# Kernel tuning notes

Measured on AMD Instinct MI355X. Metric: run time of the kernel, lower is better.

## Reference

```python
import jax, jax.numpy as jnp
import numpy as np

SR = 48000
NC = 8      # num_cylinders
NH = 64     # num_harmonics
NB = 32     # num_noisebands
B_, T_ = 2, 65536
TWO_PI = 2.0 * np.pi


def _gumbel_softmax_hard(key, logits, tau=1.0):
    g = jax.random.gumbel(key, logits.shape, dtype=logits.dtype)
    y = jax.nn.softmax((logits + g) / tau)
    hard = jax.nn.one_hot(jnp.argmax(y, axis=-1), logits.shape[-1], dtype=y.dtype)
    return hard + y - jax.lax.stop_gradient(y)  # straight-through (hard=True)


def _resonant_activation(x, min_mag):
    return jnp.sign(x) * (min_mag + (1.0 - min_mag) * jnp.abs(jnp.tanh(x)))


def _format_coefficients(one_hot, fb_gain, refl, lowpass, tau):
    shifted = jnp.roll(one_hot, 1, axis=-1)
    refl = jax.nn.sigmoid(refl) if lowpass else jnp.tanh(refl)
    k1 = _resonant_activation(refl[0], tau)
    k2 = _resonant_activation(refl[1], tau)
    a1 = k1 * (1.0 - k2)
    a2 = jnp.clip(k2, -0.999, 0.999)
    a1_bound = 0.999 - jnp.abs(a2)
    a1 = jnp.clip(a1, -a1_bound, a1_bound)
    g = jax.nn.sigmoid(fb_gain[0]) ** 0.45
    return one_hot * (a1 * g) + shifted * (a2 * g)


def _sample_wise_lpc(x, a):
    # All-pole IIR: y[t] = x[t] - sum_{i=1..P} a[t, i-1] * y[t-i]
    # x: (B,T), a: (B,T,P) -> (B,T). Inherently sequential scan over T.
    B, T = x.shape
    P = a.shape[-1]

    def step(buf, inp):          # buf: (B,P) = [y[t-1], ..., y[t-P]]
        xt, at = inp             # (B,), (B,P)
        yt = xt - jnp.sum(at * buf, axis=-1)
        buf = jnp.concatenate([yt[:, None], buf[:, :-1]], axis=1)
        return buf, yt

    buf0 = jnp.zeros((B, P), x.dtype)
    _, y = jax.lax.scan(step, buf0, (x.T, jnp.transpose(a, (1, 0, 2))))
    return y.T


def _resonator(excitation, delay_param, fb_gain, refl, min_delay, max_delay, lowpass, tau, key):
    # excitation: (B,1,T)
    sel = _gumbel_softmax_hard(key, delay_param)                 # (max-min,)
    coeffs = _format_coefficients(sel, fb_gain, refl, lowpass, tau)
    coeffs = jnp.concatenate([jnp.zeros(min_delay, coeffs.dtype), coeffs])  # (max_delay,)
    x = excitation[:, 0, :]
    B, T = x.shape
    a = jnp.broadcast_to(coeffs[None, None, :], (B, T, max_delay))
    return _sample_wise_lpc(x, a)[:, None, :]


def setup_inputs() -> dict:
    key = jax.random.key(0)
    ks = jax.random.split(key, 16)
    inp = {
        'f0': jax.random.uniform(ks[0], (B_, 1, T_), jnp.float32),
        'harmonic_amplitudes': jax.random.uniform(ks[1], (B_, NC * NH, T_), jnp.float32),
        'harmonic_fm': jax.random.uniform(ks[2], (B_, 1, T_), jnp.float32),
        'cylinder_phase_offsets': jax.random.normal(ks[3], (B_, NC, T_), jnp.float32),
        'cylinder_pulse_shapes': jax.random.uniform(ks[4], (B_, 2 * NC, T_), jnp.float32),
        'noisebank_amplitudes': jax.random.uniform(ks[5], (B_, NB, T_), jnp.float32),
        'noise_pulse_shapes': jax.random.uniform(ks[6], (B_, 2, T_), jnp.float32),
        'noise_pulse_gain': jax.random.uniform(ks[7], (B_, 1, T_), jnp.float32),
        'flow_noise_gain': jax.random.uniform(ks[8], (B_, 1, T_), jnp.float32),
        'noise_bands': jax.random.normal(ks[9], (NB, T_), jnp.float32),
        'delay_a': jax.random.normal(ks[10], (125 - 40,), jnp.float32),
        'fbgain_a': jnp.ones((1,), jnp.float32),
        'refl_a': jax.random.normal(ks[11], (2,), jnp.float32),
        'delay_b': jax.random.normal(ks[12], (125 - 40,), jnp.float32),
        'fbgain_b': jnp.ones((1,), jnp.float32),
        'refl_b': jax.random.normal(ks[13], (2,), jnp.float32),
        'delay_c': jax.random.normal(ks[14], (40 - 32,), jnp.float32),
        'fbgain_c': jnp.ones((1,), jnp.float32),
        'refl_c': jax.random.normal(ks[15], (2,), jnp.float32),
    }
    return inp


def reference(f0, harmonic_amplitudes, harmonic_fm, cylinder_phase_offsets,
              cylinder_pulse_shapes, noisebank_amplitudes, noise_pulse_shapes,
              noise_pulse_gain, flow_noise_gain, noise_bands,
              delay_a, fbgain_a, refl_a, delay_b, fbgain_b, refl_b,
              delay_c, fbgain_c, refl_c):
    B, C, T = cylinder_phase_offsets.shape
    firing_order = jnp.array([0, 4, 3, 7, 5, 2, 6, 1], dtype=f0.dtype)[:NC]
    firing_angles = firing_order / NC * TWO_PI                         # (8,)
    power_cycle_phase = jnp.cumsum(TWO_PI * f0 / SR, axis=-1) * 0.5    # (B,1,T)
    cylinder_phases = (power_cycle_phase + firing_angles[None, :, None]) % TWO_PI  # (B,8,T)

    hp = (cylinder_phases / TWO_PI) ** harmonic_fm                     # (B,8,T)
    hp = hp * TWO_PI
    harm_idx = jnp.arange(1, NH + 1, dtype=hp.dtype)
    osc = -jnp.sin(hp[:, :, None, :] * harm_idx[None, None, :, None])  # (B,8,64,T)
    amps = harmonic_amplitudes.reshape(B, NC, NH, T)
    harmonics = jnp.sum(osc * amps, axis=2)                            # (B,8,T)

    cyl_alpha = cylinder_pulse_shapes[:, :NC, :]
    cyl_beta = cylinder_pulse_shapes[:, NC:, :]
    cyl_env = (1.0 - jnp.exp(-cyl_alpha * cylinder_phases)) * jnp.exp(-cyl_beta * cylinder_phases)
    harmonics = harmonics * cyl_env * 10.0

    # NoiseBank: fixed noise bands weighted per-sample and summed over bands
    noise = jnp.einsum('bnt,nt->bt', noisebank_amplitudes, noise_bands)[:, None, :]  # (B,1,T)

    n_alpha = noise_pulse_shapes[:, 0:1, :]
    n_beta = noise_pulse_shapes[:, 1:2, :]
    noise_phase = power_cycle_phase % TWO_PI
    noise_env = (1.0 - jnp.exp(-n_alpha * noise_phase)) * jnp.exp(-n_beta * noise_phase)
    noise_bursts = noise * noise_env * noise_pulse_gain
    flow_noise = noise * flow_noise_gain * 0.3
    turbulence = harmonics * noise * (noise_pulse_gain + flow_noise_gain) * 0.7
    cylinders = harmonics + noise_bursts + flow_noise + turbulence     # (B,8,T)

    bank_a = jnp.sum(cylinders[:, :4, :], axis=1, keepdims=True)       # (B,1,T)
    bank_b = jnp.sum(cylinders[:, 4:, :], axis=1, keepdims=True)

    ka, kb, kc = jax.random.split(jax.random.key(42), 3)
    res_a = _resonator(bank_a, delay_a, fbgain_a, refl_a, 40, 125, False, 0.0, ka)
    res_b = _resonator(bank_b, delay_b, fbgain_b, refl_b, 40, 125, False, 0.0, kb)
    res_c = _resonator(res_a + res_b, delay_c, fbgain_c, refl_c, 32, 40, True, 0.0, kc)
    return jnp.sum(res_c, axis=1, keepdims=True)                       # (B,1,T)
```

## Files before the change

### kernel.cpp

```cpp
#include <hip/hip_runtime.h>
#include <cstdint>
#include <cstddef>

#define T_ 65536

__device__ __forceinline__ void tf2x32(uint32_t k0, uint32_t k1,
                                       uint32_t& x0, uint32_t& x1) {
  const uint32_t ks[3] = {k0, k1, k0 ^ k1 ^ 0x1BD11BDAu};
  const int R[8] = {13, 15, 26, 6, 17, 29, 16, 24};
  x0 += ks[0]; x1 += ks[1];
#pragma unroll
  for (int i = 0; i < 5; ++i) {
#pragma unroll
    for (int j = 0; j < 4; ++j) {
      const int r = R[(i & 1) * 4 + j];
      x0 += x1;
      x1 = (x1 << r) | (x1 >> (32 - r));
      x1 ^= x0;
    }
    x0 += ks[(i + 1) % 3];
    x1 += ks[(i + 2) % 3] + (uint32_t)(i + 1);
  }
}

__device__ __forceinline__ float gumbel_from_bits(uint32_t b) {
  float u = __uint_as_float((b >> 9) | 0x3f800000u) - 1.0f;
  u = fmaxf(u, 1.17549435e-38f);
  return -logf(-logf(u));
}

__global__ __launch_bounds__(1024) void pcp_coef_kernel(
    const float* __restrict__ f0, float* __restrict__ pcp,
    const float* __restrict__ da, const float* __restrict__ fa, const float* __restrict__ ra,
    const float* __restrict__ db, const float* __restrict__ fb, const float* __restrict__ rb,
    const float* __restrict__ dc, const float* __restrict__ fc, const float* __restrict__ rc,
    float* __restrict__ cws) {
  __shared__ double sm[1024];
  __shared__ float z[128];
  if (blockIdx.x < 2) {
    const int b = blockIdx.x;
    const int tid = threadIdx.x;
    const float* src = f0 + (size_t)b * T_;
    const int base = tid * 64;
    double loc = 0.0;
    for (int k = 0; k < 64; ++k) {
      loc += 6.283185307179586 * (double)src[base + k] / 48000.0;
    }
    sm[tid] = loc;
    __syncthreads();
    for (int off = 1; off < 1024; off <<= 1) {
      double v = (tid >= off) ? sm[tid - off] : 0.0;
      __syncthreads();
      sm[tid] += v;
      __syncthreads();
    }
    double run = (tid > 0) ? sm[tid - 1] : 0.0;
    float* dst = pcp + (size_t)b * T_;
    for (int k = 0; k < 64; ++k) {
      run += 6.283185307179586 * (double)src[base + k] / 48000.0;
      dst[base + k] = (float)(run * 0.5);
    }
  } else {
    uint32_t keys[3][2];
#pragma unroll
    for (int q = 0; q < 3; ++q) {
      uint32_t x0 = 0u, x1 = (uint32_t)q;
      tf2x32(0u, 42u, x0, x1);
      keys[q][0] = x0; keys[q][1] = x1;
    }
    const float* dl[3] = {da, db, dc};
    const float* fg[3] = {fa, fb, fc};
    const float* rf[3] = {ra, rb, rc};
    const int Ls[3] = {85, 85, 8};
    const int md[3] = {40, 40, 32};
    const int i = threadIdx.x;
    for (int r = 0; r < 3; ++r) {
      const int L = Ls[r];
      if (i < 128) z[i] = -3.4e38f;
      __syncthreads();
      if (i < L) {
        uint32_t x0 = 0u, x1 = (uint32_t)i;
        tf2x32(keys[r][0], keys[r][1], x0, x1);
        z[i] = dl[r][i] + gumbel_from_bits(x0 ^ x1);
      }
      __syncthreads();
      if (i == 0) {
        int p = 0; float best = z[0];
        for (int j = 1; j < L; ++j) { float v = z[j]; if (v > best) { best = v; p = j; } }
        const bool lowpass = (r == 2);
        float r0 = rf[r][0], r1 = rf[r][1];
        if (lowpass) { r0 = 1.f / (1.f + expf(-r0)); r1 = 1.f / (1.f + expf(-r1)); }
        else         { r0 = tanhf(r0);               r1 = tanhf(r1); }
        const float k1 = tanhf(r0), k2 = tanhf(r1);
        float a1 = k1 * (1.f - k2);
        const float a2 = fminf(fmaxf(k2, -0.999f), 0.999f);
        const float bnd = 0.999f - fabsf(a2);
        a1 = fminf(fmaxf(a1, -bnd), bnd);
        const float g = powf(1.f / (1.f + expf(-fg[r][0])), 0.45f);
        const int D1 = md[r] + p + 1;
        const int D2 = md[r] + ((p + 1) % L) + 1;
        const float C1 = a1 * g;
        const float C2 = a2 * g;
        float* cw = cws + r * 32;
        const float bin4[5] = {1.f, 4.f, 6.f, 4.f, 1.f};
        const float c1p[5] = {1.f, C1, C1*C1, C1*C1*C1, C1*C1*C1*C1};
        const float c2p[5] = {1.f, C2, C2*C2, C2*C2*C2, C2*C2*C2*C2};
        for (int j = 0; j < 5; ++j) {
          cw[j]     = (float)((4 - j) * D1 + j * D2);
          cw[5 + j] = bin4[j] * c1p[4 - j] * c2p[j];
        }
        const int   fd[9] = {D1, D2, 2*D1, D1+D2, 2*D2, 3*D1, 2*D1+D2, D1+2*D2, 3*D2};
        const float fn[9] = {-C1, -C2, C1*C1, 2.f*C1*C2, C2*C2,
                             -C1*C1*C1, -3.f*C1*C1*C2, -3.f*C1*C2*C2, -C2*C2*C2};
        for (int k = 0; k < 9; ++k) {
          cw[10 + k] = (float)fd[k];
          cw[19 + k] = fn[k];
        }
      }
      __syncthreads();
    }
  }
}

__global__ __launch_bounds__(256) void synth_kernel(
    const float* __restrict__ amps,
    const float* __restrict__ fmg,
    const float* __restrict__ cps,
    const float* __restrict__ nba,
    const float* __restrict__ nps,
    const float* __restrict__ npg,
    const float* __restrict__ fng,
    const float* __restrict__ bands,
    const float* __restrict__ pcp,
    float* __restrict__ bank_a, float* __restrict__ bank_b) {
  const float TPF = 6.283185307179586f;
  const int lane = threadIdx.x & 63;
  const int g    = threadIdx.x >> 6;
  const int blk  = blockIdx.x;
  const int b    = blk >> 8;
  const int t    = (blk & 255) * 256 + lane * 4;
  const size_t bt = (size_t)b * T_ + t;

  __shared__ float4 redN[4][64];
  __shared__ float4 redH[4][64];

  const float4 p4 = *(const float4*)(pcp + bt);
  const float4 f4 = *(const float4*)(fmg + bt);

  float4 nse = make_float4(0.f, 0.f, 0.f, 0.f);
#pragma unroll
  for (int j = 0; j < 8; ++j) {
    const int n = g * 8 + j;
    const float4 a = *(const float4*)(nba + ((size_t)b * 32 + n) * T_ + t);
    const float4 w = *(const float4*)(bands + (size_t)n * T_ + t);
    nse.x += a.x * w.x; nse.y += a.y * w.y;
    nse.z += a.z * w.z; nse.w += a.w * w.w;
  }
  redN[g][lane] = nse;

  const int order[8] = {0, 4, 3, 7, 5, 2, 6, 1};
  float4 hp = make_float4(0.f, 0.f, 0.f, 0.f);
#pragma unroll
  for (int cc = 0; cc < 2; ++cc) {
    const int c = 2 * g + cc;
    const float ang = ((float)order[c] / 8.0f) * TPF;
#define SETUP(C_)                                                     \
    float s##C_ = p4.C_ + ang; if (s##C_ >= TPF) s##C_ -= TPF;        \
    float sn##C_, cs##C_;                                             \
    sincosf(TPF * powf(s##C_ / TPF, f4.C_), &sn##C_, &cs##C_);        \
    float sp##C_ = 0.f, sc##C_ = sn##C_;                              \
    const float tc##C_ = 2.f * cs##C_;                                \
    float acc##C_ = 0.f;
    SETUP(x) SETUP(y) SETUP(z) SETUP(w)
#undef SETUP
    const float* ap = amps + ((size_t)b * 512 + (size_t)c * 64) * T_ + t;
#pragma unroll 4
    for (int h = 0; h < 64; ++h) {
      const float4 a = *(const float4*)(ap + (size_t)h * T_);
#define HSTEP(C_) {                                                   \
      acc##C_ += a.C_ * sc##C_;                                       \
      const float nx = tc##C_ * sc##C_ - sp##C_;                      \
      sp##C_ = sc##C_; sc##C_ = nx; }
      HSTEP(x) HSTEP(y) HSTEP(z) HSTEP(w)
#undef HSTEP
    }
    const float4 al = *(const float4*)(cps + ((size_t)b * 16 + c) * T_ + t);
    const float4 be = *(const float4*)(cps + ((size_t)b * 16 + 8 + c) * T_ + t);
#define ENVACC(C_) {                                                  \
      const float env = (1.f - expf(-al.C_ * s##C_)) * expf(-be.C_ * s##C_); \
      hp.C_ += -acc##C_ * env * 10.f; }
    ENVACC(x) ENVACC(y) ENVACC(z) ENVACC(w)
#undef ENVACC
  }
  redH[g][lane] = hp;
  __syncthreads();

  if (g == 0) {
    const float4 nA = redN[0][lane], nB = redN[1][lane],
                 nC = redN[2][lane], nD = redN[3][lane];
    const float4 hA0 = redH[0][lane], hA1 = redH[1][lane],
                 hB0 = redH[2][lane], hB1 = redH[3][lane];
    const float4 g4  = *(const float4*)(npg + bt);
    const float4 fl4 = *(const float4*)(fng + bt);
    const float4 na4 = *(const float4*)(nps + (size_t)b * 2 * T_ + t);
    const float4 nb4 = *(const float4*)(nps + ((size_t)b * 2 + 1) * T_ + t);
    float4 outA, outB;
#define FIN(C_) {                                                     \
    const float nse = nA.C_ + nB.C_ + nC.C_ + nD.C_;                  \
    const float ha = hA0.C_ + hA1.C_;                                 \
    const float hb = hB0.C_ + hB1.C_;                                 \
    float q = p4.C_; if (q >= TPF) q -= TPF;                          \
    const float ne = (1.f - expf(-na4.C_ * q)) * expf(-nb4.C_ * q);   \
    const float com = nse * (ne * g4.C_ + fl4.C_ * 0.3f);             \
    const float K = nse * (g4.C_ + fl4.C_) * 0.7f;                    \
    outA.C_ = ha * (1.f + K) + 4.f * com;                             \
    outB.C_ = hb * (1.f + K) + 4.f * com; }
    FIN(x) FIN(y) FIN(z) FIN(w)
#undef FIN
    *(float4*)(bank_a + bt) = outA;
    *(float4*)(bank_b + bt) = outB;
  }
}

__global__ __launch_bounds__(256) void prep_ab_kernel(
    const float* __restrict__ BA, const float* __restrict__ BB,
    const float* __restrict__ CW, float* __restrict__ XA, float* __restrict__ XB) {
  const int idx = blockIdx.x * 256 + threadIdx.x;
  const int t = idx & (T_ - 1);
  const int s = idx >> 16;
  const int r = s >> 1, b = s & 1;
  const float* xin = (r == 0 ? BA : BB) + (size_t)b * T_;
  float* xout = (r == 0 ? XA : XB) + (size_t)b * T_;
  const float* cw = CW + r * 32;
  float acc = xin[t];
#pragma unroll
  for (int k = 0; k < 9; ++k) {
    const int d = (int)cw[10 + k];
    const float n = cw[19 + k];
    const int tc = t - d;
    const float u = xin[tc >= 0 ? tc : 0];
    acc += (tc >= 0) ? n * u : 0.f;
  }
  xout[t] = acc;
}

__global__ __launch_bounds__(256) void prep_c_kernel(
    const float* __restrict__ RA, const float* __restrict__ RB,
    const float* __restrict__ CW, float* __restrict__ XC) {
  const int idx = blockIdx.x * 256 + threadIdx.x;
  const int t = idx & (T_ - 1);
  const int b = idx >> 16;
  const float* ya = RA + (size_t)b * T_;
  const float* yb = RB + (size_t)b * T_;
  const float* cw = CW + 64;
  float acc = ya[t] + yb[t];
#pragma unroll
  for (int k = 0; k < 9; ++k) {
    const int d = (int)cw[10 + k];
    const float n = cw[19 + k];
    const int tc = t - d;
    const float u = ya[tc >= 0 ? tc : 0] + yb[tc >= 0 ? tc : 0];
    acc += (tc >= 0) ? n * u : 0.f;
  }
  XC[idx] = acc;
}

__device__ __forceinline__ void gld16(const float* g, float* l) {
  __builtin_amdgcn_global_load_lds((const __attribute__((address_space(1))) void*)g,
                                   (__attribute__((address_space(3))) void*)l, 16, 0, 0);
}

__device__ __forceinline__ void poly_scan(const float* __restrict__ x,
                                          float* __restrict__ y,
                                          const float* __restrict__ cf,
                                          float* __restrict__ sm) {
  const int o = threadIdx.x & 63;
  const int e0 = (int)cf[0], e1 = (int)cf[1], e2 = (int)cf[2],
            e3 = (int)cf[3], e4 = (int)cf[4];
  const float fc0 = cf[5], fc1 = cf[6], fc2 = cf[7], fc3 = cf[8], fc4 = cf[9];
  float* ring = sm;
  float* st   = sm + 1024;

#pragma unroll
  for (int i = 0; i < 16; ++i) ring[o + i * 64] = 0.f;

#pragma unroll
  for (int seg = 0; seg < 2; ++seg) {
    const float* g = x + seg * 1024 + (o << 2);
    float* l = st + seg * 1024;
    gld16(g, l); gld16(g + 256, l + 256);
    gld16(g + 512, l + 512); gld16(g + 768, l + 768);
  }
  asm volatile("s_waitcnt vmcnt(4)" ::: "memory");

  float a0 = ring[(o - e0) & 1023];
  float a1v = ring[(o - e1) & 1023];
  float a2v = ring[(o - e2) & 1023];
  float a3v = ring[(o - e3) & 1023];
  float a4v = ring[(o - e4) & 1023];
  float b0 = ring[(o + 64 - e0) & 1023];
  float b1v = ring[(o + 64 - e1) & 1023];
  float b2v = ring[(o + 64 - e2) & 1023];
  float b3v = ring[(o + 64 - e3) & 1023];
  float b4v = ring[(o + 64 - e4) & 1023];

  int t = o;
  int bufsel = 0;
  for (int ph = 0; ph < 64; ++ph) {
    if (ph < 62) {
      const int seg = ph + 2;
      const float* g = x + seg * 1024 + (o << 2);
      float* l = st + (seg - (seg / 3) * 3) * 1024;
      gld16(g, l); gld16(g + 256, l + 256);
      gld16(g + 512, l + 512); gld16(g + 768, l + 768);
    }
    const float* bq = st + bufsel * 1024;
    bufsel = (bufsel == 2) ? 0 : (bufsel + 1);
    float xv0 = bq[o];
    float xv1 = bq[64 + o];
#pragma unroll
    for (int l = 0; l < 16; l += 2) {
      {
        const float s01 = fmaf(fc0, a0, fc1 * a1v);
        const float s23 = fmaf(fc2, a2v, fc3 * a3v);
        const float yv = xv0 + (s01 + fmaf(fc4, a4v, s23));
        ring[t & 1023] = yv;
        y[t] = yv;
        a0  = ring[(t + 128 - e0) & 1023];
        a1v = ring[(t + 128 - e1) & 1023];
        a2v = ring[(t + 128 - e2) & 1023];
        a3v = ring[(t + 128 - e3) & 1023];
        a4v = ring[(t + 128 - e4) & 1023];
        if (l + 2 < 16) xv0 = bq[(l + 2) * 64 + o];
        t += 64;
      }
      {
        const float s01 = fmaf(fc0, b0, fc1 * b1v);
        const float s23 = fmaf(fc2, b2v, fc3 * b3v);
        const float yv = xv1 + (s01 + fmaf(fc4, b4v, s23));
        ring[t & 1023] = yv;
        y[t] = yv;
        b0  = ring[(t + 128 - e0) & 1023];
        b1v = ring[(t + 128 - e1) & 1023];
        b2v = ring[(t + 128 - e2) & 1023];
        b3v = ring[(t + 128 - e3) & 1023];
        b4v = ring[(t + 128 - e4) & 1023];
        if (l + 3 < 16) xv1 = bq[(l + 3) * 64 + o];
        t += 64;
      }
    }
    asm volatile("s_waitcnt vmcnt(20)" ::: "memory");
  }
}

__global__ __launch_bounds__(64) void res_ab_kernel(
    const float* __restrict__ XA, const float* __restrict__ XB,
    float* __restrict__ RA, float* __restrict__ RB, const float* __restrict__ CW) {
  __shared__ float sm[4096];
  const int r = blockIdx.x >> 1;
  const int b = blockIdx.x & 1;
  poly_scan((r == 0 ? XA : XB) + (size_t)b * T_,
            (r == 0 ? RA : RB) + (size_t)b * T_, CW + r * 32, sm);
}

__global__ __launch_bounds__(64) void res_c_kernel(
    const float* __restrict__ XC, float* __restrict__ out,
    const float* __restrict__ CW) {
  __shared__ float sm[4096];
  poly_scan(XC + (size_t)blockIdx.x * T_, out + (size_t)blockIdx.x * T_,
            CW + 64, sm);
}

extern "C" void kernel_launch(void* const* d_in, const int* in_sizes, int n_in,
                              void* d_out, int out_size, void* d_ws, size_t ws_size,
                              hipStream_t stream) {
  const float* f0    = (const float*)d_in[0];
  const float* amps  = (const float*)d_in[1];
  const float* fmg   = (const float*)d_in[2];
  const float* cps   = (const float*)d_in[4];
  const float* nba   = (const float*)d_in[5];
  const float* nps   = (const float*)d_in[6];
  const float* npg   = (const float*)d_in[7];
  const float* fng   = (const float*)d_in[8];
  const float* bands = (const float*)d_in[9];
  const float* da  = (const float*)d_in[10];
  const float* fga = (const float*)d_in[11];
  const float* ra  = (const float*)d_in[12];
  const float* db  = (const float*)d_in[13];
  const float* fgb = (const float*)d_in[14];
  const float* rb  = (const float*)d_in[15];
  const float* dc  = (const float*)d_in[16];
  const float* fgc = (const float*)d_in[17];
  const float* rc  = (const float*)d_in[18];
  float* out = (float*)d_out;
  float* ws  = (float*)d_ws;

  float* S0 = ws;
  float* S1 = ws + 131072;
  float* S2 = ws + 262144;
  float* S3 = ws + 393216;
  float* CW = ws + 524288;

  pcp_coef_kernel<<<3, 1024, 0, stream>>>(f0, S0, da, fga, ra, db, fgb, rb,
                                          dc, fgc, rc, CW);
  synth_kernel<<<512, 256, 0, stream>>>(amps, fmg, cps, nba, nps, npg, fng, bands,
                                        S0, S1, S2);
  prep_ab_kernel<<<1024, 256, 0, stream>>>(S1, S2, CW, S0, S3);
  res_ab_kernel<<<4, 64, 0, stream>>>(S0, S3, S1, S2, CW);
  prep_c_kernel<<<512, 256, 0, stream>>>(S1, S2, CW, S3);
  res_c_kernel<<<2, 64, 0, stream>>>(S3, out, CW);
}
```

Before: 254.8 us.

## Batch scan output stores via LDS ring and vectorize phase prefix-sum loads

In the sequential resonator scan, each output was written to global memory with a scalar store on every step. Now each 1024-sample segment is collected in the LDS ring and written out as float4 stores once the segment is complete. The vmcnt wait is adjusted to match the new store count, and sched_barriers pin the instruction order. The inner loop is also rewritten to interleave the two sample streams, and the phase prefix-sum kernel now reads and writes float4. The aim is to take global store traffic and instruction count off the serial recurrence critical path, at the cost of extra LDS reads and tighter reliance on the ring layout.

```diff
diff --git a/kernel.cpp b/kernel.cpp
--- a/kernel.cpp
+++ b/kernel.cpp
@@ -43,8 +43,13 @@
     const float* src = f0 + (size_t)b * T_;
     const int base = tid * 64;
     double loc = 0.0;
-    for (int k = 0; k < 64; ++k) {
-      loc += 6.283185307179586 * (double)src[base + k] / 48000.0;
+#pragma unroll 4
+    for (int k = 0; k < 16; ++k) {
+      const float4 a = *(const float4*)(src + base + 4 * k);
+      loc += 6.283185307179586 * (double)a.x / 48000.0;
+      loc += 6.283185307179586 * (double)a.y / 48000.0;
+      loc += 6.283185307179586 * (double)a.z / 48000.0;
+      loc += 6.283185307179586 * (double)a.w / 48000.0;
     }
     sm[tid] = loc;
     __syncthreads();
@@ -56,9 +61,16 @@
     }
     double run = (tid > 0) ? sm[tid - 1] : 0.0;
     float* dst = pcp + (size_t)b * T_;
-    for (int k = 0; k < 64; ++k) {
-      run += 6.283185307179586 * (double)src[base + k] / 48000.0;
-      dst[base + k] = (float)(run * 0.5);
+#pragma unroll 4
+    for (int k = 0; k < 16; ++k) {
+      const float4 a = *(const float4*)(src + base + 4 * k);
+      const double r0 = run + 6.283185307179586 * (double)a.x / 48000.0;
+      const double r1 = r0  + 6.283185307179586 * (double)a.y / 48000.0;
+      const double r2 = r1  + 6.283185307179586 * (double)a.z / 48000.0;
+      const double r3 = r2  + 6.283185307179586 * (double)a.w / 48000.0;
+      *(float4*)(dst + base + 4 * k) = make_float4((float)(r0 * 0.5), (float)(r1 * 0.5),
+                                                   (float)(r2 * 0.5), (float)(r3 * 0.5));
+      run = r3;
     }
   } else {
     uint32_t keys[3][2];
@@ -292,6 +304,7 @@
     gld16(g + 512, l + 512); gld16(g + 768, l + 768);
   }
   asm volatile("s_waitcnt vmcnt(4)" ::: "memory");
+  __builtin_amdgcn_sched_barrier(0);
 
   float a0 = ring[(o - e0) & 1023];
   float a1v = ring[(o - e1) & 1023];
@@ -304,52 +317,46 @@
   float b3v = ring[(o + 64 - e3) & 1023];
   float b4v = ring[(o + 64 - e4) & 1023];
 
-  int t = o;
-  int bufsel = 0;
+  int m = 0;
   for (int ph = 0; ph < 64; ++ph) {
     if (ph < 62) {
       const int seg = ph + 2;
       const float* g = x + seg * 1024 + (o << 2);
-      float* l = st + (seg - (seg / 3) * 3) * 1024;
+      float* l = st + (seg % 3) * 1024;
       gld16(g, l); gld16(g + 256, l + 256);
       gld16(g + 512, l + 512); gld16(g + 768, l + 768);
     }
-    const float* bq = st + bufsel * 1024;
-    bufsel = (bufsel == 2) ? 0 : (bufsel + 1);
+    const float* bq = st + (ph % 3) * 1024;
     float xv0 = bq[o];
     float xv1 = bq[64 + o];
 #pragma unroll
-    for (int l = 0; l < 16; l += 2) {
-      {
-        const float s01 = fmaf(fc0, a0, fc1 * a1v);
-        const float s23 = fmaf(fc2, a2v, fc3 * a3v);
-        const float yv = xv0 + (s01 + fmaf(fc4, a4v, s23));
-        ring[t & 1023] = yv;
-        y[t] = yv;
-        a0  = ring[(t + 128 - e0) & 1023];
-        a1v = ring[(t + 128 - e1) & 1023];
-        a2v = ring[(t + 128 - e2) & 1023];
-        a3v = ring[(t + 128 - e3) & 1023];
-        a4v = ring[(t + 128 - e4) & 1023];
-        if (l + 2 < 16) xv0 = bq[(l + 2) * 64 + o];
-        t += 64;
-      }
-      {
-        const float s01 = fmaf(fc0, b0, fc1 * b1v);
-        const float s23 = fmaf(fc2, b2v, fc3 * b3v);
-        const float yv = xv1 + (s01 + fmaf(fc4, b4v, s23));
-        ring[t & 1023] = yv;
-        y[t] = yv;
-        b0  = ring[(t + 128 - e0) & 1023];
-        b1v = ring[(t + 128 - e1) & 1023];
-        b2v = ring[(t + 128 - e2) & 1023];
-        b3v = ring[(t + 128 - e3) & 1023];
-        b4v = ring[(t + 128 - e4) & 1023];
-        if (l + 3 < 16) xv1 = bq[(l + 3) * 64 + o];
-        t += 64;
-      }
-    }
-    asm volatile("s_waitcnt vmcnt(20)" ::: "memory");
+    for (int li = 0; li < 8; ++li) {
+      const float sA = fmaf(fc0, a0, fc1 * a1v) + fmaf(fc2, a2v, fc3 * a3v);
+      const float y0 = xv0 + fmaf(fc4, a4v, sA);
+      ring[(m + o) & 1023] = y0;
+      const float sB = fmaf(fc0, b0, fc1 * b1v) + fmaf(fc2, b2v, fc3 * b3v);
+      const float y1 = xv1 + fmaf(fc4, b4v, sB);
+      ring[(m + 64 + o) & 1023] = y1;
+      a0  = ring[(m + 128 + o - e0) & 1023];
+      a1v = ring[(m + 128 + o - e1) & 1023];
+      a2v = ring[(m + 128 + o - e2) & 1023];
+      a3v = ring[(m + 128 + o - e3) & 1023];
+      a4v = ring[(m + 128 + o - e4) & 1023];
+      b0  = ring[(m + 192 + o - e0) & 1023];
+      b1v = ring[(m + 192 + o - e1) & 1023];
+      b2v = ring[(m + 192 + o - e2) & 1023];
+      b3v = ring[(m + 192 + o - e3) & 1023];
+      b4v = ring[(m + 192 + o - e4) & 1023];
+      if (li < 7) { xv0 = bq[(li + 1) * 128 + o]; xv1 = bq[(li + 1) * 128 + 64 + o]; }
+      m += 128;
+    }
+#pragma unroll
+    for (int j = 0; j < 4; ++j) {
+      const float4 v = *(const float4*)(ring + (o << 2) + j * 256);
+      *(float4*)(y + ph * 1024 + j * 256 + (o << 2)) = v;
+    }
+    asm volatile("s_waitcnt vmcnt(8)" ::: "memory");
+    __builtin_amdgcn_sched_barrier(0);
   }
 }
 
```

After: 248.7 us. 1.02x faster.
